# Performance work log

Measured on AMD Instinct MI355X. Metric: run time of the kernel, lower is better.

## Reference

```python
import jax, jax.numpy as jnp
import numpy as np

T, N, E = 8, 50000, 800000
XD, HD, GD, ZD, TD, YHD = 128, 256, 128, 128, 8, 16
PSH = 100          # ps_predictor hidden width
BN_EPS = 1e-5


def _dense(k, fan_in, shape):
    return jax.random.normal(k, shape, jnp.float32) * (1.0 / np.sqrt(fan_in))


def setup_inputs() -> dict:
    ks = jax.random.split(jax.random.key(0), 20)
    inp = {}
    inp["X"] = jax.random.normal(ks[0], (T, N, XD), jnp.float32)
    inp["C"] = jax.random.uniform(ks[1], (T, N, TD), dtype=jnp.float32)
    inp["Y_hist"] = jax.random.normal(ks[2], (T, N, YHD), jnp.float32)
    inp["edge_index"] = jax.random.randint(ks[3], (T, 2, E), 0, N)
    # parameters
    inp["phi_W"] = _dense(ks[4], XD, (XD, HD)); inp["phi_b"] = jnp.zeros((HD,), jnp.float32)
    inp["gc_W"] = _dense(ks[5], HD, (T, HD, GD)); inp["gc_b"] = jnp.zeros((T, GD), jnp.float32)
    inp["ew_logit"] = jax.random.normal(ks[6], (T, E), jnp.float32) * 0.1  # learned edge weights (pre-sigmoid)
    inp["fuse_W"] = _dense(ks[7], 2 * HD + GD, (2 * HD + GD, ZD)); inp["fuse_b"] = jnp.zeros((ZD,), jnp.float32)
    inp["o00_W"] = _dense(ks[8], ZD, (ZD, ZD)); inp["o00_b"] = jnp.zeros((ZD,), jnp.float32)
    inp["o10_W"] = _dense(ks[9], ZD, (ZD, ZD)); inp["o10_b"] = jnp.zeros((ZD,), jnp.float32)
    inp["o01_W"] = _dense(ks[10], ZD, (ZD, 1)); inp["o01_b"] = jnp.zeros((1,), jnp.float32)
    inp["o11_W"] = _dense(ks[11], ZD, (ZD, 1)); inp["o11_b"] = jnp.zeros((1,), jnp.float32)
    inp["ps1_W"] = _dense(ks[12], ZD, (ZD, PSH)); inp["ps1_b"] = jnp.zeros((PSH,), jnp.float32)
    inp["bn_g"] = jnp.ones((PSH,), jnp.float32); inp["bn_b"] = jnp.zeros((PSH,), jnp.float32)
    inp["ps2_W"] = _dense(ks[13], PSH, (PSH, 2)); inp["ps2_b"] = jnp.zeros((2,), jnp.float32)
    inp["gru_Wih"] = _dense(ks[14], ZD + TD + YHD, (3 * HD, ZD + TD + YHD))
    inp["gru_Whh"] = _dense(ks[15], HD, (3 * HD, HD))
    inp["gru_bih"] = jnp.zeros((3 * HD,), jnp.float32)
    inp["gru_bhh"] = jnp.zeros((3 * HD,), jnp.float32)
    return inp


def reference(X, C, Y_hist, edge_index, phi_W, phi_b, gc_W, gc_b, ew_logit,
              fuse_W, fuse_b, o00_W, o00_b, o10_W, o10_b, o01_W, o01_b,
              o11_W, o11_b, ps1_W, ps1_b, bn_g, bn_b, ps2_W, ps2_b,
              gru_Wih, gru_Whh, gru_bih, gru_bhh):
    h0 = jnp.zeros((N, HD), X.dtype)
    bn_scale = bn_g / jnp.sqrt(1.0 + BN_EPS)  # eval-mode BN: running_mean=0, running_var=1

    def step(h, xs):
        x, ei, c, yh, W_t, b_t, ewl_t = xs
        phi = jax.nn.relu(x @ phi_W + phi_b)                              # [N,HD]
        # --- GCNConv with learned sigmoid edge weights + self loops ---
        src, dst = ei[0], ei[1]
        ew = jax.nn.sigmoid(ewl_t)                                        # [E]
        deg = jax.ops.segment_sum(ew, dst, num_segments=N) + 1.0          # +1 for self-loop weight
        dinv = jax.lax.rsqrt(deg)
        norm = dinv[src] * ew * dinv[dst]                                 # symmetric norm per edge
        xw = phi @ W_t                                                    # [N,GD]
        agg = jax.ops.segment_sum(norm[:, None] * xw[src], dst, num_segments=N)
        agg = agg + xw / deg[:, None] + b_t                               # self-loop contribution + bias
        rep = jax.nn.relu(agg)                                            # [N,GD] (dropout off in eval)
        # --- fuse with skip connection ---
        z = jax.nn.relu(jnp.concatenate([h, rep, phi], axis=1) @ fuse_W + fuse_b)  # [N,ZD]
        # --- GRUCell (torch gate order: reset, update, new) ---
        inp = jnp.concatenate([z, c, yh], axis=1)
        gi = inp @ gru_Wih.T + gru_bih
        gh = h @ gru_Whh.T + gru_bhh
        i_r, i_z, i_n = jnp.split(gi, 3, axis=1)
        h_r, h_z, h_n = jnp.split(gh, 3, axis=1)
        r = jax.nn.sigmoid(i_r + h_r)
        u = jax.nn.sigmoid(i_z + h_z)
        n = jnp.tanh(i_n + r * h_n)
        h_new = (1.0 - u) * n + u * h
        # --- outcome heads ---
        y0 = jax.nn.relu(z @ o00_W + o00_b) @ o01_W + o01_b               # [N,1]
        y1 = jax.nn.relu(z @ o10_W + o10_b) @ o11_W + o11_b               # [N,1]
        # --- propensity head (BatchNorm eval, sigmoid, softmax) ---
        s = jax.nn.sigmoid((z @ ps1_W + ps1_b) * bn_scale + bn_b)
        ps = jax.nn.softmax(s @ ps2_W + ps2_b, axis=1)                    # [N,2]
        return h_new, (y1, y0, z, ps)

    h_fin, (all_y1, all_y0, all_z, all_ps) = jax.lax.scan(
        step, h0, (X, edge_index, C, Y_hist, gc_W, gc_b, ew_logit))
    return all_y1, all_y0, all_z, all_ps, h_fin
```

## Files before the change

kernel.cpp:

```cpp
#include <hip/hip_runtime.h>
#include <math.h>

#define T_STEPS 8
#define NN 50000
#define EE 800000
#define TN (T_STEPS*NN)
#define TE (T_STEPS*EE)
#define GX 391

typedef unsigned int uint;
typedef unsigned short ushort;
typedef unsigned long long u64;
typedef __attribute__((ext_vector_type(8))) short short8;
typedef __attribute__((ext_vector_type(4))) float f32x4;

__device__ __forceinline__ float sigf(float x){ return 1.0f/(1.0f+expf(-x)); }
__device__ __forceinline__ ushort f2b(float f){
  uint x = __float_as_uint(f);
  uint r = (x + 0x7fffu + ((x>>16)&1u)) >> 16;
  return (ushort)r;
}
__device__ __forceinline__ float b2f(ushort u){ return __uint_as_float(((uint)u)<<16); }

__device__ __forceinline__ void gload16(const ushort* g, ushort* l){
  __builtin_amdgcn_global_load_lds(
      (const __attribute__((address_space(1))) void*)g,
      (__attribute__((address_space(3))) void*)l, 16, 0, 0);
}

template<int ROWS>
__device__ __forceinline__ void stage_tile(const ushort* base, int ld, int rowclamp,
                                           ushort* lds, int lane, int wid){
  constexpr int ITERS = ROWS/32;
#pragma unroll
  for (int i=0;i<ITERS;i++){
    int lin = i*256 + wid*64 + lane;
    int row = lin>>3, s = lin&7;
    int gr = row; if (gr > rowclamp) gr = rowclamp;
    const ushort* gp = base + (size_t)gr*ld + ((s ^ (row&7))<<3);
    gload16(gp, lds + (size_t)(i*256 + wid*64)*8);
  }
}

template<int ROWS>
__device__ __forceinline__ void stage512(const ushort* base, int ld, int rowclamp,
                                         ushort* lds, int tid){
  constexpr int ITERS = ROWS/64;
#pragma unroll
  for (int i=0;i<ITERS;i++){
    int lin = i*512 + tid;
    int row = lin>>3, s = lin&7;
    int gr = row; if (gr > rowclamp) gr = rowclamp;
    const ushort* gp = base + (size_t)gr*ld + ((s ^ (row&7))<<3);
    gload16(gp, lds + (size_t)lin*8);
  }
}

__device__ __forceinline__ short8 fragld(const ushort* lds, int R, int kk, int lane){
  int slot = (kk*4 + (lane>>4)) ^ (R&7);
  return *(const short8*)&lds[R*64 + slot*8];
}

struct Seg { const ushort* p; int ld; long ts; int w; };

__global__ __launch_bounds__(256,2) void gemm_bf(
    Seg s0, Seg s1, Seg s2,
    const ushort* __restrict__ W, int K2, long Wts,
    const float* __restrict__ bias, int act,
    const ushort* __restrict__ addp, int ldad, long adts,
    float* __restrict__ C32, int ldc, long c32ts,
    ushort* __restrict__ C16, int ldb, long c16ts,
    int Nrow, int NOvalid)
{
  __shared__ __align__(16) ushort As[8192];
  __shared__ __align__(16) ushort Bs[8192];
  const int t    = blockIdx.z;
  const int tid  = threadIdx.x;
  const int lane = tid & 63;
  const int wid  = __builtin_amdgcn_readfirstlane(tid >> 6);
  const int brow = blockIdx.x*128;
  const int bcol = blockIdx.y*128;
  const int wr = wid>>1, wc = wid&1;

  f32x4 acc[4][4];
#pragma unroll
  for(int m=0;m<4;m++)
#pragma unroll
    for(int n=0;n<4;n++) acc[m][n] = (f32x4){0.f,0.f,0.f,0.f};

  const int nk = K2 >> 6;
  for (int kt=0; kt<nk; ++kt){
    int col0 = kt*64;
    const ushort* ab; int ald;
    if (col0 < s0.w){ ab = s0.p + (size_t)t*s0.ts + col0; ald = s0.ld; }
    else if (col0 < s0.w + s1.w){ ab = s1.p + (size_t)t*s1.ts + (col0 - s0.w); ald = s1.ld; }
    else { ab = s2.p + (size_t)t*s2.ts + (col0 - s0.w - s1.w); ald = s2.ld; }
    stage_tile<128>(ab + (size_t)brow*ald, ald, Nrow-1-brow, As, lane, wid);
    stage_tile<128>(W + (size_t)t*Wts + (size_t)bcol*K2 + col0, K2, 1<<30, Bs, lane, wid);
    __syncthreads();
#pragma unroll
    for (int kk=0;kk<2;kk++){
      short8 a[4], b[4];
#pragma unroll
      for (int m=0;m<4;m++) a[m] = fragld(As, wr*64 + m*16 + (lane&15), kk, lane);
#pragma unroll
      for (int n=0;n<4;n++) b[n] = fragld(Bs, wc*64 + n*16 + (lane&15), kk, lane);
#pragma unroll
      for (int m=0;m<4;m++)
#pragma unroll
        for (int n=0;n<4;n++)
          acc[m][n] = __builtin_amdgcn_mfma_f32_16x16x32_bf16(a[m], b[n], acc[m][n], 0,0,0);
    }
    __syncthreads();
  }
  const int rbase = brow + wr*64 + (lane>>4)*4;
  const int cbase = bcol + wc*64 + (lane&15);
#pragma unroll
  for (int m=0;m<4;m++){
#pragma unroll
    for (int q=0;q<4;q++){
      int r = rbase + m*16 + q;
      if (r >= Nrow) continue;
#pragma unroll
      for (int n=0;n<4;n++){
        int c = cbase + n*16;
        if (c >= NOvalid) continue;
        float v = acc[m][n][q];
        if (addp) v += b2f(addp[(size_t)t*adts + (size_t)r*ldad + c]);
        if (bias) v += bias[c];
        if (act==1) v = fmaxf(v, 0.f);
        if (C32) C32[(size_t)t*c32ts + (size_t)r*ldc + c] = v;
        if (C16) C16[(size_t)t*c16ts + (size_t)r*ldb + c] = f2b(v);
      }
    }
  }
}

__global__ __launch_bounds__(512,2) void gemm_phi512(
    const float* __restrict__ A32,
    const ushort* __restrict__ W,
    const float* __restrict__ bias,
    ushort* __restrict__ C16, long c16ts,
    int Nrow)
{
  __shared__ __align__(16) ushort As[8192];
  __shared__ __align__(16) ushort Bs[16384];
  const int t    = blockIdx.z;
  const int tid  = threadIdx.x;
  const int lane = tid & 63;
  const int wid  = __builtin_amdgcn_readfirstlane(tid >> 6);
  const int brow = blockIdx.x*128;
  const int wr = wid>>2, wc = wid&3;
  const float* At = A32 + (size_t)t*NN*128;

  f32x4 acc[4][4];
#pragma unroll
  for(int m=0;m<4;m++)
#pragma unroll
    for(int n=0;n<4;n++) acc[m][n] = (f32x4){0.f,0.f,0.f,0.f};

  for (int kt=0; kt<2; ++kt){
    int col0 = kt*64;
#pragma unroll
    for (int it=0; it<4; ++it){
      int lin = it*512 + tid;
      int row = lin>>4, q4 = lin&15;
      int grow = brow + row; if (grow >= Nrow) grow = Nrow-1;
      float4 v = *(const float4*)&At[(size_t)grow*128 + col0 + q4*4];
      int s = q4>>1, half = q4&1;
      uint lo = (uint)f2b(v.x) | ((uint)f2b(v.y)<<16);
      uint hi = (uint)f2b(v.z) | ((uint)f2b(v.w)<<16);
      *(uint2*)&As[row*64 + ((s ^ (row&7))<<3) + half*4] = make_uint2(lo,hi);
    }
    stage512<256>(W + col0, 128, 1<<30, Bs, tid);
    __syncthreads();
#pragma unroll
    for (int kk=0;kk<2;kk++){
      short8 a[4], b[4];
#pragma unroll
      for (int m=0;m<4;m++) a[m] = fragld(As, wr*64 + m*16 + (lane&15), kk, lane);
#pragma unroll
      for (int n=0;n<4;n++) b[n] = fragld(Bs, wc*64 + n*16 + (lane&15), kk, lane);
#pragma unroll
      for (int m=0;m<4;m++)
#pragma unroll
        for (int n=0;n<4;n++)
          acc[m][n] = __builtin_amdgcn_mfma_f32_16x16x32_bf16(a[m], b[n], acc[m][n], 0,0,0);
    }
    __syncthreads();
  }
  const int rbase = brow + wr*64 + (lane>>4)*4;
  const int cbase = wc*64 + (lane&15);
#pragma unroll
  for (int m=0;m<4;m++){
#pragma unroll
    for (int q=0;q<4;q++){
      int r = rbase + m*16 + q;
      if (r >= Nrow) continue;
#pragma unroll
      for (int n=0;n<4;n++){
        int c = cbase + n*16;
        float v = acc[m][n][q] + bias[c];
        v = fmaxf(v, 0.f);
        C16[(size_t)t*c16ts + (size_t)r*256 + c] = f2b(v);
      }
    }
  }
}

__global__ __launch_bounds__(512,2) void gemm_gru512(
    Seg s0, Seg s1, Seg s2,
    const ushort* __restrict__ W,
    const float* __restrict__ bg,
    const float* __restrict__ hin,
    float* __restrict__ hout, ushort* __restrict__ hbfo,
    int Nrow)
{
  __shared__ __align__(16) ushort As[8192];
  __shared__ __align__(16) ushort Bs[16384];
  const int tid  = threadIdx.x;
  const int lane = tid & 63;
  const int wid  = __builtin_amdgcn_readfirstlane(tid >> 6);
  const int brow = blockIdx.x*128;
  const int bcol = blockIdx.y*256;
  const int wr = wid>>2, wc = wid&3;
  const int K2 = 448;

  f32x4 acc[4][4];
#pragma unroll
  for(int m=0;m<4;m++)
#pragma unroll
    for(int n=0;n<4;n++) acc[m][n] = (f32x4){0.f,0.f,0.f,0.f};

  for (int kt=0; kt<7; ++kt){
    int col0 = kt*64;
    const ushort* ab; int ald;
    if (col0 < s0.w){ ab = s0.p + col0; ald = s0.ld; }
    else if (col0 < s0.w + s1.w){ ab = s1.p + (col0 - s0.w); ald = s1.ld; }
    else { ab = s2.p + (col0 - s0.w - s1.w); ald = s2.ld; }
    stage512<128>(ab + (size_t)brow*ald, ald, Nrow-1-brow, As, tid);
    stage512<256>(W + (size_t)bcol*K2 + col0, K2, 1<<30, Bs, tid);
    __syncthreads();
#pragma unroll
    for (int kk=0;kk<2;kk++){
      short8 a[4], b[4];
#pragma unroll
      for (int m=0;m<4;m++) a[m] = fragld(As, wr*64 + m*16 + (lane&15), kk, lane);
#pragma unroll
      for (int n=0;n<4;n++) b[n] = fragld(Bs, wc*64 + n*16 + (lane&15), kk, lane);
#pragma unroll
      for (int m=0;m<4;m++)
#pragma unroll
        for (int n=0;n<4;n++)
          acc[m][n] = __builtin_amdgcn_mfma_f32_16x16x32_bf16(a[m], b[n], acc[m][n], 0,0,0);
    }
    __syncthreads();
  }
  const int jj = lane&15;
  const int G  = blockIdx.y*4 + wc;
  const int j  = G*16 + jj;
  const int rbase = brow + wr*64 + (lane>>4)*4;
  float bb[4];
#pragma unroll
  for (int n=0;n<4;n++) bb[n] = bg[G*64 + n*16 + jj];
#pragma unroll
  for (int m=0;m<4;m++){
#pragma unroll
    for (int q=0;q<4;q++){
      int r = rbase + m*16 + q;
      if (r >= Nrow) continue;
      float v0 = acc[m][0][q] + bb[0];
      float v1 = acc[m][1][q] + bb[1];
      float v2 = acc[m][2][q] + bb[2];
      float v3 = acc[m][3][q] + bb[3];
      float rg = sigf(v0), ug = sigf(v1);
      float ng = tanhf(v2 + rg*v3);
      float ho = hin[(size_t)r*256 + j];
      float hn = (1.f-ug)*ng + ug*ho;
      hout[(size_t)r*256 + j] = hn;
      hbfo[(size_t)r*256 + j] = f2b(hn);
    }
  }
}

__global__ __launch_bounds__(256,2) void heads_k(
    const ushort* __restrict__ Az, long Ats,
    const ushort* __restrict__ W,
    const float* __restrict__ o00b, const float* __restrict__ o10b,
    const float* __restrict__ w01, const float* __restrict__ b01,
    const float* __restrict__ w11, const float* __restrict__ b11,
    float* __restrict__ y0out, long y0ts,
    float* __restrict__ y1out, long y1ts, int Nrow)
{
  __shared__ __align__(16) ushort As[4096];
  __shared__ __align__(16) ushort Bs[16384];
  __shared__ float shy[4][64];
  const int t    = blockIdx.z;
  const int tid  = threadIdx.x;
  const int lane = tid & 63;
  const int wid  = __builtin_amdgcn_readfirstlane(tid >> 6);
  const int brow = blockIdx.x*64;
  const ushort* A = Az + (size_t)t*Ats;

  f32x4 acc[4][4];
#pragma unroll
  for(int m=0;m<4;m++)
#pragma unroll
    for(int n=0;n<4;n++) acc[m][n] = (f32x4){0.f,0.f,0.f,0.f};

  for (int kt=0; kt<2; ++kt){
    stage_tile<64>(A + (size_t)brow*128 + kt*64, 128, Nrow-1-brow, As, lane, wid);
    stage_tile<256>(W + kt*64, 128, 1<<30, Bs, lane, wid);
    __syncthreads();
#pragma unroll
    for (int kk=0;kk<2;kk++){
      short8 a[4], b[4];
#pragma unroll
      for (int m=0;m<4;m++) a[m] = fragld(As, m*16 + (lane&15), kk, lane);
#pragma unroll
      for (int n=0;n<4;n++) b[n] = fragld(Bs, wid*64 + n*16 + (lane&15), kk, lane);
#pragma unroll
      for (int m=0;m<4;m++)
#pragma unroll
        for (int n=0;n<4;n++)
          acc[m][n] = __builtin_amdgcn_mfma_f32_16x16x32_bf16(a[m], b[n], acc[m][n], 0,0,0);
    }
    __syncthreads();
  }
  float bb[4], ww[4];
#pragma unroll
  for (int n=0;n<4;n++){
    int c = wid*64 + n*16 + (lane&15);
    bb[n] = (c<128)? o00b[c] : o10b[c-128];
    ww[n] = (c<128)? w01[c]  : w11[c-128];
  }
#pragma unroll
  for (int m=0;m<4;m++){
#pragma unroll
    for (int q=0;q<4;q++){
      float p = 0.f;
#pragma unroll
      for (int n=0;n<4;n++) p += fmaxf(acc[m][n][q] + bb[n], 0.f) * ww[n];
#pragma unroll
      for (int o=1;o<16;o<<=1) p += __shfl_xor(p, o);
      if ((lane&15)==0) shy[wid][m*16 + (lane>>4)*4 + q] = p;
    }
  }
  __syncthreads();
  if (tid < 64){
    int r = brow + tid;
    if (r < Nrow){
      y0out[(size_t)t*y0ts + r] = shy[0][tid] + shy[1][tid] + b01[0];
      y1out[(size_t)t*y1ts + r] = shy[2][tid] + shy[3][tid] + b11[0];
    }
  }
}

__global__ __launch_bounds__(256,2) void ps_k(
    const ushort* __restrict__ Az, long Ats,
    const ushort* __restrict__ W,
    const float* __restrict__ psc, const float* __restrict__ psb,
    const float* __restrict__ W2, const float* __restrict__ b2,
    float* __restrict__ psout, long psts, int Nrow)
{
  __shared__ __align__(16) ushort As[8192];
  __shared__ __align__(16) ushort Bs[8192];
  __shared__ float sh0[2][128];
  __shared__ float sh1[2][128];
  const int t    = blockIdx.z;
  const int tid  = threadIdx.x;
  const int lane = tid & 63;
  const int wid  = __builtin_amdgcn_readfirstlane(tid >> 6);
  const int brow = blockIdx.x*128;
  const int wr = wid>>1, wc = wid&1;
  const ushort* A = Az + (size_t)t*Ats;

  f32x4 acc[4][4];
#pragma unroll
  for(int m=0;m<4;m++)
#pragma unroll
    for(int n=0;n<4;n++) acc[m][n] = (f32x4){0.f,0.f,0.f,0.f};

  for (int kt=0; kt<2; ++kt){
    stage_tile<128>(A + (size_t)brow*128 + kt*64, 128, Nrow-1-brow, As, lane, wid);
    stage_tile<128>(W + kt*64, 128, 1<<30, Bs, lane, wid);
    __syncthreads();
#pragma unroll
    for (int kk=0;kk<2;kk++){
      short8 a[4], b[4];
#pragma unroll
      for (int m=0;m<4;m++) a[m] = fragld(As, wr*64 + m*16 + (lane&15), kk, lane);
#pragma unroll
      for (int n=0;n<4;n++) b[n] = fragld(Bs, wc*64 + n*16 + (lane&15), kk, lane);
#pragma unroll
      for (int m=0;m<4;m++)
#pragma unroll
        for (int n=0;n<4;n++)
          acc[m][n] = __builtin_amdgcn_mfma_f32_16x16x32_bf16(a[m], b[n], acc[m][n], 0,0,0);
    }
    __syncthreads();
  }
  float sc[4], sb[4], w0_[4], w1_[4];
#pragma unroll
  for (int n=0;n<4;n++){
    int c = wc*64 + n*16 + (lane&15);
    bool ok = (c<100);
    sc[n] = ok? psc[c] : 0.f;
    sb[n] = ok? psb[c] : 0.f;
    w0_[n]= ok? W2[2*c] : 0.f;
    w1_[n]= ok? W2[2*c+1] : 0.f;
  }
#pragma unroll
  for (int m=0;m<4;m++){
#pragma unroll
    for (int q=0;q<4;q++){
      float a0=0.f, a1=0.f;
#pragma unroll
      for (int n=0;n<4;n++){
        float s = sigf(acc[m][n][q]*sc[n] + sb[n]);
        a0 += s*w0_[n]; a1 += s*w1_[n];
      }
#pragma unroll
      for (int o=1;o<16;o<<=1){ a0 += __shfl_xor(a0,o); a1 += __shfl_xor(a1,o); }
      if ((lane&15)==0){
        int rt = wr*64 + m*16 + (lane>>4)*4 + q;
        sh0[wc][rt] = a0; sh1[wc][rt] = a1;
      }
    }
  }
  __syncthreads();
  if (tid < 128){
    int r = brow + tid;
    if (r < Nrow){
      float l0 = sh0[0][tid]+sh0[1][tid]+b2[0];
      float l1 = sh1[0][tid]+sh1[1][tid]+b2[1];
      float mx = fmaxf(l0,l1);
      float e0 = expf(l0-mx), e1 = expf(l1-mx);
      float inv = 1.f/(e0+e1);
      psout[(size_t)t*psts + (size_t)r*2]   = e0*inv;
      psout[(size_t)t*psts + (size_t)r*2+1] = e1*inv;
    }
  }
}

__global__ void count_k(const int* __restrict__ ei, const float* __restrict__ ewl,
                        uint* __restrict__ degcnt, ushort* __restrict__ rank)
{
  int idx = blockIdx.x*256 + threadIdx.x;
  if (idx >= TE) return;
  int t = idx / EE;
  int e = idx - t*EE;
  const int* dst = ei + (size_t)t*2*EE + EE;
  int d = dst[e];
  uint v = (1u<<24) | (uint)(sigf(ewl[idx]) * 262144.0f);
  uint old = atomicAdd(&degcnt[t*NN + d], v);
  rank[idx] = (ushort)(old>>24);
}

__global__ void dinv_k(const uint* __restrict__ degcnt, int* __restrict__ cnt,
                       float* __restrict__ dnv, float* __restrict__ invd){
  int idx = blockIdx.x*256+threadIdx.x;
  if (idx>=TN) return;
  uint tot = degcnt[idx];
  int c = (int)(tot>>24);
  float S = (float)(tot & 0xFFFFFFu) * (1.f/262144.f);
  float dv = S + 1.f;
  cnt[idx] = c;
  dnv[idx]  = rsqrtf(dv);
  invd[idx] = 1.f/dv;
}

__global__ void scan1_k(const int* __restrict__ in, int* __restrict__ outv,
                        int* __restrict__ partials, int n)
{
  __shared__ int sh[256];
  int base = blockIdx.x*1024;
  int tid = threadIdx.x;
  int v[4]; int s=0;
#pragma unroll
  for (int i=0;i<4;i++){ int idx=base+tid*4+i; v[i] = (idx<n)? in[idx]:0; s+=v[i]; }
  sh[tid]=s; __syncthreads();
  for (int o=1;o<256;o<<=1){
    int t2 = (tid>=o)? sh[tid-o]:0;
    __syncthreads();
    sh[tid]+=t2;
    __syncthreads();
  }
  int excl = sh[tid]-s;
#pragma unroll
  for (int i=0;i<4;i++){ int idx=base+tid*4+i; if(idx<n) outv[idx]=excl; excl+=v[i]; }
  if (tid==255) partials[blockIdx.x]=sh[255];
}

__global__ void scan2_k(int* p, int np){
  __shared__ int sh[256];
  __shared__ int run;
  int tid=threadIdx.x;
  if(tid==0) run=0;
  __syncthreads();
  for(int base=0;base<np;base+=256){
    int v = (base+tid<np)? p[base+tid]:0;
    sh[tid]=v; __syncthreads();
    for(int o=1;o<256;o<<=1){
      int t2 = (tid>=o)? sh[tid-o]:0;
      __syncthreads();
      sh[tid]+=t2;
      __syncthreads();
    }
    int incl=sh[tid];
    int r0=run;
    __syncthreads();
    if(base+tid<np) p[base+tid]=r0+incl-v;
    __syncthreads();
    if(tid==0) run = r0 + sh[255];
    __syncthreads();
  }
}

__global__ void scan3_k(int* __restrict__ offs, const int* __restrict__ parts, int n){
  int idx = blockIdx.x*256+threadIdx.x;
  if (idx==0) offs[n] = TE;
  if (idx<n){ offs[idx] = offs[idx] + parts[idx>>10]; }
}

__global__ void fill_k(const int* __restrict__ ei, const float* __restrict__ ewl,
                       const float* __restrict__ dnv, const int* __restrict__ offs,
                       const ushort* __restrict__ rank, uint* __restrict__ epack)
{
  int idx = blockIdx.x*256 + threadIdx.x;
  if (idx >= TE) return;
  int t = idx / EE;
  int e = idx - t*EE;
  const int* srcp = ei + (size_t)t*2*EE;
  const int* dstp = srcp + EE;
  int s=srcp[e], d=dstp[e];
  float nr = dnv[t*NN+s] * sigf(ewl[idx]) * dnv[t*NN+d];
  uint nq = (uint)(nr*65535.f + 0.5f);
  int pos = offs[t*NN+d] + rank[idx];
  epack[pos] = (uint)s | (nq<<16);
}

__global__ __launch_bounds__(256) void gather_k(const int* __restrict__ offs,
    const uint* __restrict__ epack,
    const ushort* __restrict__ xwb, const float* __restrict__ invd,
    const float* __restrict__ gcb, ushort* __restrict__ rep)
{
  int bid  = blockIdx.x;
  int t    = bid & 7;
  int node = (bid>>3)*4 + (threadIdx.x>>6);
  int lane = threadIdx.x & 63;
  int half = lane>>5, ll = lane&31;
  if (node >= NN) return;
  const int* offs_t = offs + (size_t)t*NN;
  const ushort* xw_t = xwb + (size_t)t*NN*128;
  int o0 = offs_t[node], o1 = offs_t[node+1];
  float a0=0.f, a1=0.f, a2=0.f, a3=0.f;

#define ACC4(nv, uv) \
    a0 = fmaf(nv, __uint_as_float((uv).x<<16),          a0); \
    a1 = fmaf(nv, __uint_as_float((uv).x & 0xffff0000u), a1); \
    a2 = fmaf(nv, __uint_as_float((uv).y<<16),          a2); \
    a3 = fmaf(nv, __uint_as_float((uv).y & 0xffff0000u), a3);

  int j = o0 + half;
  for (; j+6 < o1; j += 8){
    uint e0 = epack[j],   e1 = epack[j+2];
    uint e2 = epack[j+4], e3 = epack[j+6];
    uint2 v0 = ((const uint2*)(xw_t + (size_t)(e0&0xffff)*128))[ll];
    uint2 v1 = ((const uint2*)(xw_t + (size_t)(e1&0xffff)*128))[ll];
    uint2 v2 = ((const uint2*)(xw_t + (size_t)(e2&0xffff)*128))[ll];
    uint2 v3 = ((const uint2*)(xw_t + (size_t)(e3&0xffff)*128))[ll];
    float n0 = (float)(e0>>16), n1 = (float)(e1>>16);
    float n2 = (float)(e2>>16), n3 = (float)(e3>>16);
    ACC4(n0, v0)
    ACC4(n1, v1)
    ACC4(n2, v2)
    ACC4(n3, v3)
  }
  for (; j < o1; j += 2){
    uint e0 = epack[j];
    uint2 v0 = ((const uint2*)(xw_t + (size_t)(e0&0xffff)*128))[ll];
    float n0 = (float)(e0>>16);
    ACC4(n0, v0)
  }
#undef ACC4
  a0 += __shfl_xor(a0, 32);
  a1 += __shfl_xor(a1, 32);
  a2 += __shfl_xor(a2, 32);
  a3 += __shfl_xor(a3, 32);
  const float qs = 1.f/65535.f;
  a0 *= qs; a1 *= qs; a2 *= qs; a3 *= qs;
  float sl = invd[(size_t)t*NN + node];
  uint2 us = ((const uint2*)(xw_t + (size_t)node*128))[ll];
  float4 gb = ((const float4*)(gcb + (size_t)t*128))[ll];
  a0 = fmaf(sl, __uint_as_float(us.x<<16),           a0) + gb.x;
  a1 = fmaf(sl, __uint_as_float(us.x & 0xffff0000u), a1) + gb.y;
  a2 = fmaf(sl, __uint_as_float(us.y<<16),           a2) + gb.z;
  a3 = fmaf(sl, __uint_as_float(us.y & 0xffff0000u), a3) + gb.w;
  a0 = fmaxf(a0,0.f); a1 = fmaxf(a1,0.f);
  a2 = fmaxf(a2,0.f); a3 = fmaxf(a3,0.f);
  if (half==0){
    uint pk0 = (uint)f2b(a0) | ((uint)f2b(a1)<<16);
    uint pk1 = (uint)f2b(a2) | ((uint)f2b(a3)<<16);
    ((uint2*)(rep + ((size_t)t*NN + node)*128))[ll] = make_uint2(pk0, pk1);
  }
}

__global__ __launch_bounds__(256) void prep_k(
    const float* __restrict__ phiW, const float* __restrict__ gcW,
    const float* __restrict__ fuseW, const float* __restrict__ ps1W,
    const float* __restrict__ Wih, const float* __restrict__ Whh,
    const float* __restrict__ bih, const float* __restrict__ bhh,
    const float* __restrict__ o00W, const float* __restrict__ o10W,
    const float* __restrict__ ps1b, const float* __restrict__ bng,
    const float* __restrict__ bnb,
    ushort* __restrict__ phiWt, ushort* __restrict__ gcWt,
    ushort* __restrict__ WhT, ushort* __restrict__ WrpT,
    ushort* __restrict__ ps1T, ushort* __restrict__ Wg,
    float* __restrict__ bg, ushort* __restrict__ wocT,
    float* __restrict__ psc, float* __restrict__ psb)
{
  const int bid = blockIdx.x;
  const int tid = threadIdx.x;
  if (bid < 128){
    int idx = bid*256 + tid;
    int o = idx>>7, k = idx&127;
    phiWt[idx] = f2b(phiW[(size_t)k*256 + o]);
  } else if (bid < 1152){
    int idx = (bid-128)*256 + tid;
    int t = idx>>15, rem = idx&32767, o = rem>>8, k = rem&255;
    gcWt[idx] = f2b(gcW[(size_t)t*32768 + (size_t)k*128 + o]);
  } else if (bid < 1280){
    int idx = (bid-1152)*256 + tid;
    int o = idx>>8, k = idx&255;
    WhT[idx] = f2b(fuseW[(size_t)k*128 + o]);
  } else if (bid < 1472){
    int idx = (bid-1280)*256 + tid;
    int o = idx/384, k = idx - o*384;
    WrpT[idx] = f2b(fuseW[32768 + (size_t)k*128 + o]);
  } else if (bid < 1536){
    int idx = (bid-1472)*256 + tid;
    int o = idx>>7, k = idx&127;
    ps1T[idx] = f2b((o<100)? ps1W[(size_t)k*100 + o] : 0.f);
  } else if (bid < 3328){
    int idx = (bid-1536)*256 + tid;
    int c = idx/448, k = idx - c*448;
    int G = c>>6, g = (c>>4)&3, jj = c&15;
    int j = G*16 + jj;
    float v = 0.f;
    if (k < 152){
      if      (g==0) v = Wih[(size_t)j*152 + k];
      else if (g==1) v = Wih[(size_t)(256+j)*152 + k];
      else if (g==2) v = Wih[(size_t)(512+j)*152 + k];
    } else if (k >= 192){
      int kk = k-192;
      if      (g==0) v = Whh[(size_t)j*256 + kk];
      else if (g==1) v = Whh[(size_t)(256+j)*256 + kk];
      else if (g==3) v = Whh[(size_t)(512+j)*256 + kk];
    }
    Wg[idx] = f2b(v);
    if (k==0){
      float b;
      if      (g==0) b = bih[j]     + bhh[j];
      else if (g==1) b = bih[256+j] + bhh[256+j];
      else if (g==2) b = bih[512+j];
      else           b = bhh[512+j];
      bg[c] = b;
    }
  } else if (bid < 3456){
    int idx = (bid-3328)*256 + tid;
    int o = idx>>7, k = idx&127;
    float v = (o<128) ? o00W[(size_t)k*128 + o] : o10W[(size_t)k*128 + (o-128)];
    wocT[idx] = f2b(v);
  } else {
    int i = tid;
    if (i<100){ float sc = bng[i]*rsqrtf(1.f+1e-5f); psc[i]=sc; psb[i]=ps1b[i]*sc+bnb[i]; }
    else if (i<128){ psc[i]=0.f; psb[i]=0.f; }
  }
}

__global__ void cyh_k(ushort* __restrict__ cyh, const float* __restrict__ Cc,
                      const float* __restrict__ Yh)
{
  long gid = (long)blockIdx.x*256 + threadIdx.x;
  if (gid >= (long)TN*64) return;
  long g = gid >> 6; int l = (int)(gid & 63);
  float v = 0.f;
  if (l < 8)       v = Cc[g*8 + l];
  else if (l < 24) v = Yh[g*16 + (l-8)];
  cyh[g*64 + l] = f2b(v);
}

extern "C" void kernel_launch(void* const* d_in, const int* in_sizes, int n_in,
                              void* d_out_v, int out_size, void* d_ws, size_t ws_size,
                              hipStream_t stream)
{
  const float* X    = (const float*)d_in[0];
  const float* Cc   = (const float*)d_in[1];
  const float* Yh   = (const float*)d_in[2];
  const int*   EI   = (const int*)  d_in[3];
  const float* phiW = (const float*)d_in[4];  const float* phib = (const float*)d_in[5];
  const float* gcW  = (const float*)d_in[6];  const float* gcb  = (const float*)d_in[7];
  const float* ewl  = (const float*)d_in[8];
  const float* fuseW= (const float*)d_in[9];  const float* fuseb= (const float*)d_in[10];
  const float* o00W = (const float*)d_in[11]; const float* o00b = (const float*)d_in[12];
  const float* o10W = (const float*)d_in[13]; const float* o10b = (const float*)d_in[14];
  const float* o01W = (const float*)d_in[15]; const float* o01b = (const float*)d_in[16];
  const float* o11W = (const float*)d_in[17]; const float* o11b = (const float*)d_in[18];
  const float* ps1W = (const float*)d_in[19]; const float* ps1b = (const float*)d_in[20];
  const float* bng  = (const float*)d_in[21]; const float* bnb  = (const float*)d_in[22];
  const float* ps2W = (const float*)d_in[23]; const float* ps2b = (const float*)d_in[24];
  const float* Wih  = (const float*)d_in[25]; const float* Whh  = (const float*)d_in[26];
  const float* bih  = (const float*)d_in[27]; const float* bhh  = (const float*)d_in[28];
  float* out = (float*)d_out_v;

  char* wsb = (char*)d_ws;
  size_t off=0;
  auto alloc=[&](size_t bytes)->void*{
    void* p = wsb + off;
    off = (off + bytes + 255) & ~(size_t)255;
    return p;
  };
  uint*  degcnt= (uint*) alloc((size_t)TN*4);
  int*   cnt   = (int*)  alloc((size_t)TN*4);
  int*   offs  = (int*)  alloc(((size_t)TN+1)*4);
  float* dnv   = (float*)alloc((size_t)TN*4);
  float* invd  = (float*)alloc((size_t)TN*4);
  uint*  epack = (uint*) alloc((size_t)TE*4);
  ushort* rankb= (ushort*)alloc((size_t)TE*2);
  int*   parts = (int*)  alloc(4096);
  ushort* rep_all = (ushort*)alloc((size_t)TN*128*2);
  ushort* phiA = (ushort*)alloc((size_t)TN*256*2);
  ushort* xwb  = (ushort*)alloc((size_t)TN*128*2);
  ushort* pz   = (ushort*)alloc((size_t)TN*128*2);
  ushort* hbf0 = (ushort*)alloc((size_t)NN*256*2);
  ushort* hbf1 = (ushort*)alloc((size_t)NN*256*2);
  float*  hb   = (float*)alloc((size_t)NN*256*4);
  ushort* phiWt= (ushort*)alloc(256*128*2);
  ushort* gcWt = (ushort*)alloc((size_t)T_STEPS*128*256*2);
  ushort* WhT  = (ushort*)alloc(128*256*2);
  ushort* WrpT = (ushort*)alloc(128*384*2);
  ushort* Wgru = (ushort*)alloc((size_t)1024*448*2);
  float* bgru  = (float*)alloc(1024*4);
  ushort* wocT = (ushort*)alloc(256*128*2);
  ushort* ps1T = (ushort*)alloc(128*128*2);
  float* psc   = (float*)alloc(128*4);
  float* psb   = (float*)alloc(128*4);

  ushort* zbf     = phiA;
  ushort* cyh     = phiA + (size_t)TN*128;

  hipMemsetAsync(degcnt, 0, (size_t)TN*4, stream);
  hipMemsetAsync(hb,   0, (size_t)NN*256*4, stream);
  hipMemsetAsync(hbf0, 0, (size_t)NN*256*2, stream);

  prep_k<<<3457,256,0,stream>>>(phiW, gcW, fuseW, ps1W, Wih, Whh, bih, bhh,
    o00W, o10W, ps1b, bng, bnb,
    phiWt, gcWt, WhT, WrpT, ps1T, Wgru, bgru, wocT, psc, psb);

  count_k<<<(TE+255)/256,256,0,stream>>>(EI,ewl,degcnt,rankb);
  dinv_k<<<(TN+255)/256,256,0,stream>>>(degcnt,cnt,dnv,invd);
  scan1_k<<<(TN+1023)/1024,256,0,stream>>>(cnt,offs,parts,TN);
  scan2_k<<<1,256,0,stream>>>(parts,(TN+1023)/1024);
  scan3_k<<<(TN+255)/256,256,0,stream>>>(offs,parts,TN);
  fill_k<<<(TE+255)/256,256,0,stream>>>(EI,ewl,dnv,offs,rankb,epack);

  const size_t zoff  = (size_t)2*TN;
  const size_t psoff = zoff + (size_t)TN*128;
  const size_t hoff  = psoff + (size_t)TN*2;
  const Seg S0 = {nullptr,0,0,0};

  gemm_phi512<<<dim3(GX,1,8),512,0,stream>>>(
    X, phiWt, phib, phiA, (long)NN*256, NN);
  gemm_bf<<<dim3(GX,1,8),256,0,stream>>>(
    Seg{phiA,256,(long)NN*256,256}, S0, S0, gcWt,256,(long)128*256, nullptr,0,
    nullptr,0,0, nullptr,0,0, xwb,128,(long)NN*128, NN,128);
  gather_k<<<(NN/4)*8,256,0,stream>>>(offs, epack, xwb, invd, gcb, rep_all);
  gemm_bf<<<dim3(GX,1,8),256,0,stream>>>(
    Seg{rep_all,128,(long)NN*128,128}, Seg{phiA,256,(long)NN*256,256}, S0,
    WrpT,384,0, nullptr,0,
    nullptr,0,0, nullptr,0,0, pz,128,(long)NN*128, NN,128);
  cyh_k<<<(int)(((long)TN*64+255)/256),256,0,stream>>>(cyh, Cc, Yh);

  for (int t=0;t<T_STEPS;t++){
    const ushort* hbi = (t&1)? hbf1 : hbf0;
    ushort*       hbo = (t&1)? hbf0 : hbf1;
    float* hout = (t==T_STEPS-1)? (out+hoff) : hb;
    float* zt = out + zoff + (size_t)t*NN*128;
    ushort* zbt = zbf + (size_t)t*NN*128;
    gemm_bf<<<dim3(GX,1,1),256,0,stream>>>(
      Seg{hbi,256,0,256}, S0, S0, WhT,256,0, fuseb,1,
      pz + (size_t)t*NN*128,128,0, zt,128,0, zbt,128,0, NN,128);
    gemm_gru512<<<dim3(GX,4),512,0,stream>>>(
      Seg{zbt,128,0,128}, Seg{cyh + (size_t)t*NN*64,64,0,64}, Seg{hbi,256,0,256},
      Wgru, bgru, hb, hout, hbo, NN);
  }

  heads_k<<<dim3((NN+63)/64,1,8),256,0,stream>>>(
    zbf,(long)NN*128, wocT, o00b,o10b, o01W,o01b, o11W,o11b,
    out + TN, (long)NN,
    out, (long)NN, NN);
  ps_k<<<dim3(GX,1,8),256,0,stream>>>(
    zbf,(long)NN*128, ps1T, psc,psb, ps2W,ps2b,
    out+psoff, (long)NN*2, NN);

  (void)in_sizes; (void)n_in; (void)out_size; (void)ws_size;
}
```

Measured before the change: 2.283 ms.

## Fuse fusion-layer z GEMM into GRU GEMM kernel via shared memory

Each GRU GEMM block now computes its 128-row slice of z (h @ WhT + precomputed part + bias, ReLU) into shared memory and uses it directly as the first K-tiles of the gate GEMM. This removes the separate z kernel launch per timestep and the z reload from global memory. In exchange, every column block recomputes the same z tile, about four times redundant work, and shared memory use grows, which may reduce occupancy.

Result: slower. 2.847 ms (+24.7%).

```diff
diff --git a/kernel.cpp b/kernel.cpp
--- a/kernel.cpp
+++ b/kernel.cpp
@@ -208,23 +208,80 @@
   }
 }
 
-__global__ __launch_bounds__(512,2) void gemm_gru512(
-    Seg s0, Seg s1, Seg s2,
-    const ushort* __restrict__ W,
-    const float* __restrict__ bg,
-    const float* __restrict__ hin,
+__global__ __launch_bounds__(512,2) void gemm_gruz(
+    const ushort* __restrict__ hbf,
+    const ushort* __restrict__ pzt,
+    const float*  __restrict__ fuseb,
+    const ushort* __restrict__ WhT,
+    const ushort* __restrict__ cyht,
+    const ushort* __restrict__ Wg,
+    const float*  __restrict__ bg,
+    const float*  __restrict__ hin,
     float* __restrict__ hout, ushort* __restrict__ hbfo,
+    float* __restrict__ zt32, ushort* __restrict__ zbft,
     int Nrow)
 {
   __shared__ __align__(16) ushort As[8192];
   __shared__ __align__(16) ushort Bs[16384];
+  __shared__ __align__(16) ushort Zs[16384];
   const int tid  = threadIdx.x;
   const int lane = tid & 63;
   const int wid  = __builtin_amdgcn_readfirstlane(tid >> 6);
   const int brow = blockIdx.x*128;
   const int bcol = blockIdx.y*256;
   const int wr = wid>>2, wc = wid&3;
-  const int K2 = 448;
+
+  {
+    f32x4 zacc[4][2];
+#pragma unroll
+    for(int m=0;m<4;m++)
+#pragma unroll
+      for(int n=0;n<2;n++) zacc[m][n] = (f32x4){0.f,0.f,0.f,0.f};
+    for (int kt=0; kt<4; ++kt){
+      int col0 = kt*64;
+      stage512<128>(hbf + (size_t)brow*256 + col0, 256, Nrow-1-brow, As, tid);
+      stage512<128>(WhT + col0, 256, 1<<30, Bs, tid);
+      __syncthreads();
+#pragma unroll
+      for (int kk=0;kk<2;kk++){
+        short8 a[4], b[2];
+#pragma unroll
+        for (int m=0;m<4;m++) a[m] = fragld(As, wr*64 + m*16 + (lane&15), kk, lane);
+#pragma unroll
+        for (int n=0;n<2;n++) b[n] = fragld(Bs, wc*32 + n*16 + (lane&15), kk, lane);
+#pragma unroll
+        for (int m=0;m<4;m++)
+#pragma unroll
+          for (int n=0;n<2;n++)
+            zacc[m][n] = __builtin_amdgcn_mfma_f32_16x16x32_bf16(a[m], b[n], zacc[m][n], 0,0,0);
+      }
+      __syncthreads();
+    }
+    const int rl0 = wr*64 + (lane>>4)*4;
+#pragma unroll
+    for (int m=0;m<4;m++){
+#pragma unroll
+      for (int q=0;q<4;q++){
+        int rloc = rl0 + m*16 + q;
+        int r = brow + rloc;
+        if (r >= Nrow) continue;
+#pragma unroll
+        for (int n=0;n<2;n++){
+          int c = wc*32 + n*16 + (lane&15);
+          float v = zacc[m][n][q] + b2f(pzt[(size_t)r*128 + c]) + fuseb[c];
+          v = fmaxf(v, 0.f);
+          ushort hv = f2b(v);
+          int sub = c>>6, cp = c&63, sp = cp>>3, j2 = cp&7;
+          Zs[sub*8192 + rloc*64 + ((sp ^ (rloc&7))<<3) + j2] = hv;
+          if (blockIdx.y==0){
+            zt32[(size_t)r*128 + c] = v;
+            zbft[(size_t)r*128 + c] = hv;
+          }
+        }
+      }
+    }
+  }
+  __syncthreads();
 
   f32x4 acc[4][4];
 #pragma unroll
@@ -233,19 +290,18 @@
     for(int n=0;n<4;n++) acc[m][n] = (f32x4){0.f,0.f,0.f,0.f};
 
   for (int kt=0; kt<7; ++kt){
-    int col0 = kt*64;
-    const ushort* ab; int ald;
-    if (col0 < s0.w){ ab = s0.p + col0; ald = s0.ld; }
-    else if (col0 < s0.w + s1.w){ ab = s1.p + (col0 - s0.w); ald = s1.ld; }
-    else { ab = s2.p + (col0 - s0.w - s1.w); ald = s2.ld; }
-    stage512<128>(ab + (size_t)brow*ald, ald, Nrow-1-brow, As, tid);
-    stage512<256>(W + (size_t)bcol*K2 + col0, K2, 1<<30, Bs, tid);
-    __syncthreads();
+    if (kt == 2)
+      stage512<128>(cyht + (size_t)brow*64, 64, Nrow-1-brow, As, tid);
+    else if (kt >= 3)
+      stage512<128>(hbf + (size_t)brow*256 + (kt-3)*64, 256, Nrow-1-brow, As, tid);
+    stage512<256>(Wg + (size_t)bcol*448 + kt*64, 448, 1<<30, Bs, tid);
+    __syncthreads();
+    const ushort* asrc = (kt<2) ? (Zs + kt*8192) : As;
 #pragma unroll
     for (int kk=0;kk<2;kk++){
       short8 a[4], b[4];
 #pragma unroll
-      for (int m=0;m<4;m++) a[m] = fragld(As, wr*64 + m*16 + (lane&15), kk, lane);
+      for (int m=0;m<4;m++) a[m] = fragld(asrc, wr*64 + m*16 + (lane&15), kk, lane);
 #pragma unroll
       for (int n=0;n<4;n++) b[n] = fragld(Bs, wc*64 + n*16 + (lane&15), kk, lane);
 #pragma unroll
@@ -788,12 +844,9 @@
     float* hout = (t==T_STEPS-1)? (out+hoff) : hb;
     float* zt = out + zoff + (size_t)t*NN*128;
     ushort* zbt = zbf + (size_t)t*NN*128;
-    gemm_bf<<<dim3(GX,1,1),256,0,stream>>>(
-      Seg{hbi,256,0,256}, S0, S0, WhT,256,0, fuseb,1,
-      pz + (size_t)t*NN*128,128,0, zt,128,0, zbt,128,0, NN,128);
-    gemm_gru512<<<dim3(GX,4),512,0,stream>>>(
-      Seg{zbt,128,0,128}, Seg{cyh + (size_t)t*NN*64,64,0,64}, Seg{hbi,256,0,256},
-      Wgru, bgru, hb, hout, hbo, NN);
+    gemm_gruz<<<dim3(GX,4),512,0,stream>>>(
+      hbi, pz + (size_t)t*NN*128, fuseb, WhT, cyh + (size_t)t*NN*64,
+      Wgru, bgru, hb, hout, hbo, zt, zbt, NN);
   }
 
   heads_k<<<dim3((NN+63)/64,1,8),256,0,stream>>>(
```
